# Optimization experiments

Measured on AMD Instinct MI355X. Metric: run time of the kernel, lower is better.

Reference implementation:

```python
import jax, jax.numpy as jnp
import numpy as np

N, E, F_IN, E_DIM, H, G = 8192, 40960, 32, 8, 64, 64
EPS = 1e-5


def _lin(key, fan_in, fan_out):
    k1, k2 = jax.random.split(key)
    s = 1.0 / np.sqrt(fan_in)
    w = jax.random.uniform(k1, (fan_in, fan_out), jnp.float32, -s, s)
    b = jax.random.uniform(k2, (fan_out,), jnp.float32, -s, s)
    return w, b


def setup_inputs() -> dict:
    key = jax.random.key(0)
    ks = jax.random.split(key, 32)
    inp = {}
    inp['x'] = jax.random.normal(ks[0], (N, F_IN), jnp.float32)
    inp['edge_index'] = jax.random.randint(ks[1], (2, E), 0, N)
    inp['edge_attr'] = jax.random.normal(ks[2], (E, E_DIM), jnp.float32)
    inp['batch'] = jnp.sort(jax.random.randint(ks[3], (N,), 0, G))
    # NNConv 1 (F_IN -> H)
    inp['e1_w1'], inp['e1_b1'] = _lin(ks[4], E_DIM, H)
    inp['e1_w2'], inp['e1_b2'] = _lin(ks[5], H, F_IN * H)
    inp['root1_w'], inp['root1_b'] = _lin(ks[6], F_IN, H)
    inp['bn1_g'] = jnp.ones((H,), jnp.float32); inp['bn1_b'] = jnp.zeros((H,), jnp.float32)
    # NNConv 2 (H -> H)
    inp['e2_w1'], inp['e2_b1'] = _lin(ks[7], E_DIM, H)
    inp['e2_w2'], inp['e2_b2'] = _lin(ks[8], H, H * H)
    inp['root2_w'], inp['root2_b'] = _lin(ks[9], H, H)
    inp['bn2_g'] = jnp.ones((H,), jnp.float32); inp['bn2_b'] = jnp.zeros((H,), jnp.float32)
    # NNConv 3 (H -> H)
    inp['e3_w1'], inp['e3_b1'] = _lin(ks[10], E_DIM, H)
    inp['e3_w2'], inp['e3_b2'] = _lin(ks[11], H, H * H)
    inp['root3_w'], inp['root3_b'] = _lin(ks[12], H, H)
    inp['bn3_g'] = jnp.ones((H,), jnp.float32); inp['bn3_b'] = jnp.zeros((H,), jnp.float32)
    # attention gate MLP: H -> H//2 -> 1
    inp['gate_w1'], inp['gate_b1'] = _lin(ks[13], H, H // 2)
    inp['gate_w2'], inp['gate_b2'] = _lin(ks[14], H // 2, 1)
    # fc head: H -> 2H (BN, relu) -> H (BN, relu) -> 1
    inp['fc1_w'], inp['fc1_b'] = _lin(ks[15], H, 2 * H)
    inp['fcbn1_g'] = jnp.ones((2 * H,), jnp.float32); inp['fcbn1_b'] = jnp.zeros((2 * H,), jnp.float32)
    inp['fc2_w'], inp['fc2_b'] = _lin(ks[16], 2 * H, H)
    inp['fcbn2_g'] = jnp.ones((H,), jnp.float32); inp['fcbn2_b'] = jnp.zeros((H,), jnp.float32)
    inp['fc3_w'], inp['fc3_b'] = _lin(ks[17], H, 1)
    return inp


def _bn(x, g, b):
    # training-mode batch norm over node/graph dim
    m = jnp.mean(x, axis=0)
    v = jnp.var(x, axis=0)
    return (x - m) * jax.lax.rsqrt(v + EPS) * g + b


def _nnconv(x, edge_index, edge_attr, w1, b1, w2, b2, root_w, root_b, in_ch, out_ch):
    src, dst = edge_index[0], edge_index[1]
    h = jax.nn.relu(edge_attr @ w1 + b1)                     # [E, H]
    We = (h @ w2 + b2).reshape(-1, in_ch, out_ch)            # [E, in, out]
    msg = jnp.einsum('ei,eio->eo', x[src], We)               # [E, out]
    s = jax.ops.segment_sum(msg, dst, num_segments=N)
    cnt = jax.ops.segment_sum(jnp.ones((msg.shape[0],), x.dtype), dst, num_segments=N)
    agg = s / jnp.clip(cnt, 1.0)[:, None]                    # mean aggregation
    return agg + x @ root_w + root_b


def _global_attention(x, batch, gw1, gb1, gw2, gb2):
    gate = jax.nn.relu(x @ gw1 + gb1) @ gw2 + gb2            # [N, 1]
    gate = gate[:, 0]
    m = jax.ops.segment_max(gate, batch, num_segments=G)
    e = jnp.exp(gate - m[batch])
    z = jax.ops.segment_sum(e, batch, num_segments=G)
    alpha = e / z[batch]
    return jax.ops.segment_sum(alpha[:, None] * x, batch, num_segments=G)  # [G, H]


def reference(x, edge_index, edge_attr, batch,
              e1_w1, e1_b1, e1_w2, e1_b2, root1_w, root1_b, bn1_g, bn1_b,
              e2_w1, e2_b1, e2_w2, e2_b2, root2_w, root2_b, bn2_g, bn2_b,
              e3_w1, e3_b1, e3_w2, e3_b2, root3_w, root3_b, bn3_g, bn3_b,
              gate_w1, gate_b1, gate_w2, gate_b2,
              fc1_w, fc1_b, fcbn1_g, fcbn1_b, fc2_w, fc2_b, fcbn2_g, fcbn2_b, fc3_w, fc3_b):
    x1 = jax.nn.relu(_bn(_nnconv(x, edge_index, edge_attr, e1_w1, e1_b1, e1_w2, e1_b2, root1_w, root1_b, F_IN, H), bn1_g, bn1_b))
    x2 = jax.nn.relu(_bn(_nnconv(x1, edge_index, edge_attr, e2_w1, e2_b1, e2_w2, e2_b2, root2_w, root2_b, H, H), bn2_g, bn2_b)) + x1
    x3 = jax.nn.relu(_bn(_nnconv(x2, edge_index, edge_attr, e3_w1, e3_b1, e3_w2, e3_b2, root3_w, root3_b, H, H), bn3_g, bn3_b)) + x2
    # dropout is identity in eval/reference mode
    p = _global_attention(x3, batch, gate_w1, gate_b1, gate_w2, gate_b2)  # [G, H]
    h = jax.nn.relu(_bn(p @ fc1_w + fc1_b, fcbn1_g, fcbn1_b))
    h = jax.nn.relu(_bn(h @ fc2_w + fc2_b, fcbn2_g, fcbn2_b))
    out = h @ fc3_w + fc3_b
    return out[:, 0]
```

## Files before the change

### kernel.cpp

```cpp
#include <hip/hip_runtime.h>
#include <hip/hip_bf16.h>

#define NN 8192
#define EE 40960
#define FIN 32
#define HH 64
#define GG 64

typedef __attribute__((ext_vector_type(4))) float f32x4;
typedef __attribute__((ext_vector_type(8))) short s16x8;
typedef unsigned short ushort_t;

__device__ __forceinline__ unsigned short f2bf(float f) {
    union { float f; unsigned int u; } v; v.f = f;
    unsigned int u = v.u;
    return (unsigned short)((u + 0x7fffu + ((u >> 16) & 1u)) >> 16);
}

__device__ __forceinline__ void gll16(const void* g, void* l) {
    __builtin_amdgcn_global_load_lds((__attribute__((address_space(1))) void*)g,
                                     (__attribute__((address_space(3))) void*)l, 16, 0, 0);
}

__global__ void btbuild_all_kernel(const float* __restrict__ w2a, const float* __restrict__ b2a, ushort_t* __restrict__ Bta,
                                   const float* __restrict__ w2b, const float* __restrict__ b2b, ushort_t* __restrict__ Btb,
                                   const float* __restrict__ w2c, const float* __restrict__ b2c, ushort_t* __restrict__ Btc,
                                   int* __restrict__ cnt, int* __restrict__ fill, float* __restrict__ stats,
                                   const float* __restrict__ x, const float* __restrict__ r1w,
                                   const float* __restrict__ r1b, float* __restrict__ rootbuf) {
    int bid = blockIdx.x;
    int t = threadIdx.x;

    if (bid >= 2600) {
        __shared__ float xs[16][36];
        __shared__ float rws[32 * 64];
        __shared__ float rbs[64];
        int blk = bid - 2600;
        for (int j = t; j < 512; j += 256) { int r = j >> 5, i = j & 31; xs[r][i] = x[(size_t)(blk * 16 + r) * 32 + i]; }
        for (int i = t; i < 2048; i += 256) rws[i] = r1w[i];
        if (t < 64) rbs[t] = r1b[t];
        __syncthreads();
        int r = t >> 4, cg = (t & 15) * 4;
        f32x4 s = *(const f32x4*)&rbs[cg];
#pragma unroll 8
        for (int i = 0; i < 32; i++) {
            float xv = xs[r][i];
            s += xv * (*(const f32x4*)&rws[i * 64 + cg]);
        }
        *(f32x4*)&rootbuf[(size_t)(blk * 16 + r) * 64 + cg] = s;
        return;
    }

    if (bid < 32) { cnt[bid * 256 + t] = 0; fill[bid * 256 + t] = 0; }
    if (bid == 32) stats[t] = 0.f;
    if (bid == 33 && t < 128) stats[256 + t] = 0.f;

    const float* w2; const float* b2; ushort_t* Bt; int IC; int base;
    if (bid < 520)       { w2 = w2a; b2 = b2a; Bt = Bta; IC = 32; base = bid; }
    else if (bid < 1560) { w2 = w2b; b2 = b2b; Bt = Btb; IC = 64; base = bid - 520; }
    else                 { w2 = w2c; b2 = b2c; Bt = Btc; IC = 64; base = bid - 1560; }
    int CH = IC >> 3;
    int flat = base * 256 + t;
    if (flat >= 64 * 65 * IC) return;
    int s = flat / (64 * IC);
    int rem = flat - s * (64 * IC);
    int row = rem / IC;
    int j = rem - row * IC;
    int q = j >> 3, w = j & 7;
    int c = q ^ (row & (CH - 1));
    int i = c * 8 + w;
    float v = (s < 64) ? w2[s * (IC * 64) + i * 64 + row] : b2[i * 64 + row];
    Bt[flat] = f2bf(v);
}

__global__ void hist_kernel(const int* __restrict__ dst, int* __restrict__ cnt) {
    int e = blockIdx.x * 256 + threadIdx.x;
    if (e < EE) atomicAdd(&cnt[dst[e]], 1);
}

__global__ void scan_kernel(const int* __restrict__ cnt, int* __restrict__ row_ptr) {
    __shared__ int lds[1024];
    int t = threadIdx.x;
    int v[8]; int s = 0;
    int base = t * 8;
#pragma unroll
    for (int j = 0; j < 8; j++) { v[j] = s; s += cnt[base + j]; }
    lds[t] = s;
    __syncthreads();
    for (int off = 1; off < 1024; off <<= 1) {
        int add = (t >= off) ? lds[t - off] : 0;
        __syncthreads();
        lds[t] += add;
        __syncthreads();
    }
    int ex = lds[t] - s;
#pragma unroll
    for (int j = 0; j < 8; j++) row_ptr[base + j] = ex + v[j];
    if (t == 1023) row_ptr[NN] = lds[1023];
}

__global__ void scatter_kernel(const int* __restrict__ dst, const int* __restrict__ row_ptr,
                               int* __restrict__ fill, int* __restrict__ perm) {
    int e = blockIdx.x * 256 + threadIdx.x;
    if (e < EE) {
        int d = dst[e];
        int pos = row_ptr[d] + atomicAdd(&fill[d], 1);
        perm[pos] = e;
    }
}

template<int IC>
__launch_bounds__(256, 5)
__global__ void conv_msg_kernel(const float* __restrict__ eattr,
                                const float* __restrict__ w1,
                                const float* __restrict__ b1,
                                const float* __restrict__ xin,
                                const int* __restrict__ src,
                                const int* __restrict__ perm,
                                const ushort_t* __restrict__ Bt,
                                float* __restrict__ msg) {
    constexpr int NKK  = IC / 32;
    constexpr int CH   = IC / 8;
    constexpr int TILE = IC * 64;
    constexpr int NQ   = (TILE * 2) / 4096;
    __shared__ ushort_t bt_lds[2][TILE];
    __shared__ float h_t[2048];
    __shared__ float ea_s[32][9];
    __shared__ float w1s[512];
    __shared__ float b1s[64];
    __shared__ int eid_s[32];

    const int t = threadIdx.x;
    const int wave = t >> 6;
    const int l = t & 63;
    const int g = l >> 4;
    const int rlo = l & 15;
    const int e0 = blockIdx.x * 32;

    auto stage = [&](int buf, int step) {
#pragma unroll
        for (int q = 0; q < NQ; ++q) {
            int off = q * 2048 + wave * 512;
            const ushort_t* gp = Bt + (size_t)step * TILE + off + l * 8;
            gll16(gp, &bt_lds[buf][off]);
        }
    };

    stage(0, 0);

    if (t < 32) eid_s[t] = perm[e0 + t];
    if (t < 64) b1s[t] = b1[t];
    for (int i = t; i < 512; i += 256) w1s[i] = w1[i];
    __syncthreads();

    { int e = t >> 3, i = t & 7; ea_s[e][i] = eattr[(size_t)eid_s[e] * 8 + i]; }

    s16x8 afrag[2][NKK];
#pragma unroll
    for (int m = 0; m < 2; ++m) {
        int row = m * 16 + rlo;
        int sn = src[eid_s[row]];
        const float* xp = xin + (size_t)sn * IC + g * 8;
#pragma unroll
        for (int kk = 0; kk < NKK; ++kk) {
            f32x4 a = *(const f32x4*)(xp + kk * 32);
            f32x4 b = *(const f32x4*)(xp + kk * 32 + 4);
            s16x8 fr;
            fr[0] = (short)f2bf(a[0]); fr[1] = (short)f2bf(a[1]);
            fr[2] = (short)f2bf(a[2]); fr[3] = (short)f2bf(a[3]);
            fr[4] = (short)f2bf(b[0]); fr[5] = (short)f2bf(b[1]);
            fr[6] = (short)f2bf(b[2]); fr[7] = (short)f2bf(b[3]);
            afrag[m][kk] = fr;
        }
    }
    __syncthreads();

#pragma unroll
    for (int j = 0; j < 8; ++j) {
        int idx = t + 256 * j;
        int k = idx >> 5, e = idx & 31;
        float s = b1s[k];
#pragma unroll
        for (int i = 0; i < 8; i++) s += ea_s[e][i] * w1s[i * 64 + k];
        h_t[idx] = fmaxf(s, 0.f);
    }
    __syncthreads();

    f32x4 acc[2];
#pragma unroll
    for (int m = 0; m < 2; m++) acc[m] = (f32x4){0.f, 0.f, 0.f, 0.f};

    const int bcol = wave * 16 + rlo;
    const int bmask = bcol & (CH - 1);
    const f32x4 zf = (f32x4){0.f, 0.f, 0.f, 0.f};

    for (int step = 0; step < 65; ++step) {
        if (step < 64) stage((step + 1) & 1, step + 1);
        const int buf = step & 1;
        s16x8 bfr[NKK];
#pragma unroll
        for (int kk = 0; kk < NKK; kk++) {
            int q = (kk * 4 + g) ^ bmask;
            bfr[kk] = *(const s16x8*)&bt_lds[buf][bcol * IC + q * 8];
        }
#pragma unroll
        for (int m = 0; m < 2; m++) {
            f32x4 P = __builtin_amdgcn_mfma_f32_16x16x32_bf16(afrag[m][0], bfr[0], zf, 0, 0, 0);
            if constexpr (NKK == 2)
                P = __builtin_amdgcn_mfma_f32_16x16x32_bf16(afrag[m][1], bfr[1], P, 0, 0, 0);
            if (step == 64) {
                acc[m] += P;
            } else {
                f32x4 h4 = *(const f32x4*)&h_t[(step << 5) + m * 16 + (g << 2)];
                acc[m] += h4 * P;
            }
        }
        __syncthreads();
    }

#pragma unroll
    for (int m = 0; m < 2; m++) {
        int row = e0 + m * 16 + (g << 2);
        float* mp = msg + (size_t)row * 64 + wave * 16 + rlo;
        mp[0] = acc[m][0]; mp[64] = acc[m][1]; mp[128] = acc[m][2]; mp[192] = acc[m][3];
    }
}

__global__ void aggregate_kernel(const float* __restrict__ msg, const int* __restrict__ row_ptr,
                                 const float* __restrict__ rootbuf,
                                 float* __restrict__ y, float* __restrict__ stats) {
    int t = threadIdx.x;
    int n = blockIdx.x * 16 + (t >> 4);
    int cg = (t & 15) * 4;
    int s = row_ptr[n], e = row_ptr[n + 1];
    f32x4 acc = (f32x4){0.f, 0.f, 0.f, 0.f};
    for (int j = s; j < e; ++j) {
        acc += *(const f32x4*)&msg[(size_t)j * 64 + cg];
    }
    float inv = 1.0f / fmaxf((float)(e - s), 1.0f);
    acc *= inv;
    acc += *(const f32x4*)&rootbuf[(size_t)n * 64 + cg];
    *(f32x4*)&y[(size_t)n * 64 + cg] = acc;

    f32x4 a2 = acc * acc;
#pragma unroll
    for (int j = 0; j < 4; j++) {
        acc[j] += __shfl_xor(acc[j], 16); acc[j] += __shfl_xor(acc[j], 32);
        a2[j]  += __shfl_xor(a2[j], 16);  a2[j]  += __shfl_xor(a2[j], 32);
    }
    __shared__ float ls[4][64], lq[4][64];
    int w = t >> 6;
    if ((t & 63) < 16) {
#pragma unroll
        for (int j = 0; j < 4; j++) { ls[w][cg + j] = acc[j]; lq[w][cg + j] = a2[j]; }
    }
    __syncthreads();
    if (t < 64) {
        float S = ls[0][t] + ls[1][t] + ls[2][t] + ls[3][t];
        float Q = lq[0][t] + lq[1][t] + lq[2][t] + lq[3][t];
        atomicAdd(&stats[t], S);
        atomicAdd(&stats[64 + t], Q);
    }
}

__global__ void bn_apply_root_kernel(const float* __restrict__ y, const float* __restrict__ stats,
                                     const float* __restrict__ gam, const float* __restrict__ bet,
                                     const float* __restrict__ res, float* __restrict__ xout,
                                     const float* __restrict__ rw, const float* __restrict__ rb,
                                     float* __restrict__ rootbuf) {
    __shared__ float xs[16][68];
    __shared__ float rws[64 * 64];
    __shared__ float rbs[64];
    int t = threadIdx.x;
    for (int i = t; i < 4096; i += 256) rws[i] = rw[i];
    if (t < 64) rbs[t] = rb[t];
    int i4 = blockIdx.x * 256 + t;
    int row = t >> 4, cg = (t & 15) * 4;
    const float invN = 1.0f / (float)NN;
    f32x4 yv = *(const f32x4*)&y[(size_t)i4 * 4];
    f32x4 o;
#pragma unroll
    for (int j = 0; j < 4; j++) {
        int c = cg + j;
        float mean = stats[c] * invN;
        float var = stats[64 + c] * invN - mean * mean;
        float sc = rsqrtf(var + 1e-5f) * gam[c];
        o[j] = fmaxf((yv[j] - mean) * sc + bet[c], 0.f);
    }
    if (res) o += *(const f32x4*)&res[(size_t)i4 * 4];
    *(f32x4*)&xout[(size_t)i4 * 4] = o;
    *(f32x4*)&xs[row][cg] = o;
    __syncthreads();
    f32x4 s = *(const f32x4*)&rbs[cg];
#pragma unroll 8
    for (int i = 0; i < 64; i++) {
        float xv = xs[row][i];
        s += xv * (*(const f32x4*)&rws[i * 64 + cg]);
    }
    *(f32x4*)&rootbuf[(size_t)(blockIdx.x * 16 + row) * 64 + cg] = s;
}

__global__ void bn_gate_kernel(const float* __restrict__ y, const float* __restrict__ stats,
                               const float* __restrict__ gam, const float* __restrict__ bet,
                               const float* __restrict__ res, float* __restrict__ xout,
                               const float* __restrict__ gw1, const float* __restrict__ gb1,
                               const float* __restrict__ gw2, const float* __restrict__ gb2,
                               float* __restrict__ gate) {
    __shared__ float x3s[64][68];
    __shared__ float w1s[2048];
    __shared__ float b1s[32], w2s[32];
    __shared__ float b2s;
    int t = threadIdx.x;
    for (int i = t; i < 2048; i += 256) w1s[i] = gw1[i];
    if (t < 32) { b1s[t] = gb1[t]; w2s[t] = gw2[t]; }
    if (t == 0) b2s = gb2[0];
    const float invN = 1.0f / (float)NN;
    size_t base4 = (size_t)blockIdx.x * 1024;
#pragma unroll
    for (int j = 0; j < 4; j++) {
        int i4l = j * 256 + t;
        int row = i4l >> 4, cg = (i4l & 15) * 4;
        f32x4 yv = *(const f32x4*)&y[(base4 + i4l) * 4];
        f32x4 o;
#pragma unroll
        for (int jj = 0; jj < 4; jj++) {
            int c = cg + jj;
            float mean = stats[c] * invN;
            float var = stats[64 + c] * invN - mean * mean;
            float sc = rsqrtf(var + 1e-5f) * gam[c];
            o[jj] = fmaxf((yv[jj] - mean) * sc + bet[c], 0.f);
        }
        o += *(const f32x4*)&res[(base4 + i4l) * 4];
        *(f32x4*)&xout[(base4 + i4l) * 4] = o;
        *(f32x4*)&x3s[row][cg] = o;
    }
    __syncthreads();
    int w = t >> 6, l = t & 63;
    int row = w * 16 + (l >> 2), part = l & 3;
    float hacc[8];
#pragma unroll
    for (int j = 0; j < 8; j++) hacc[j] = b1s[part * 8 + j];
    for (int i = 0; i < 64; i++) {
        float xv = x3s[row][i];
#pragma unroll
        for (int j = 0; j < 8; j++) hacc[j] += xv * w1s[i * 32 + part * 8 + j];
    }
    float gv = 0.f;
#pragma unroll
    for (int j = 0; j < 8; j++) gv += fmaxf(hacc[j], 0.f) * w2s[part * 8 + j];
    gv += __shfl_xor(gv, 1); gv += __shfl_xor(gv, 2);
    if (part == 0) gate[blockIdx.x * 64 + row] = gv + b2s;
}

__global__ void attn_pool_kernel(const float* __restrict__ x3, const float* __restrict__ gate,
                                 const int* __restrict__ batch, float* __restrict__ p) {
    int g = blockIdx.x;
    int t = threadIdx.x;
    int lo = 0, hi = NN;
    while (lo < hi) { int mid = (lo + hi) >> 1; if (batch[mid] < g) lo = mid + 1; else hi = mid; }
    int s = lo;
    hi = NN;
    while (lo < hi) { int mid = (lo + hi) >> 1; if (batch[mid] < g + 1) lo = mid + 1; else hi = mid; }
    int e = lo;

    __shared__ float red[4];
    __shared__ float sM, sZ;
    float m = -1e30f;
    for (int n = s + t; n < e; n += 256) m = fmaxf(m, gate[n]);
#pragma unroll
    for (int off = 1; off < 64; off <<= 1) m = fmaxf(m, __shfl_xor(m, off));
    if ((t & 63) == 0) red[t >> 6] = m;
    __syncthreads();
    if (t == 0) sM = fmaxf(fmaxf(red[0], red[1]), fmaxf(red[2], red[3]));
    __syncthreads();
    float z = 0.f;
    for (int n = s + t; n < e; n += 256) z += __expf(gate[n] - sM);
#pragma unroll
    for (int off = 1; off < 64; off <<= 1) z += __shfl_xor(z, off);
    if ((t & 63) == 0) red[t >> 6] = z;
    __syncthreads();
    if (t == 0) sZ = red[0] + red[1] + red[2] + red[3];
    __syncthreads();
    int w = t >> 6, c = t & 63;
    float acc = 0.f;
    for (int n = s + w; n < e; n += 4) acc += __expf(gate[n] - sM) * x3[(size_t)n * 64 + c];
    __shared__ float pa[4][64];
    pa[w][c] = acc;
    __syncthreads();
    if (t < 64) {
        float v = pa[0][t] + pa[1][t] + pa[2][t] + pa[3][t];
        p[g * 64 + t] = (sZ > 0.f) ? v / sZ : 0.f;
    }
}

__global__ void head1_kernel(const float* __restrict__ p, const float* __restrict__ fc1w,
                             const float* __restrict__ fc1b, const float* __restrict__ bn1g,
                             const float* __restrict__ bn1b, float* __restrict__ t1n) {
    __shared__ float sp[64 * 65];
    __shared__ float w1s[64 * 16];
    __shared__ float t1s[64 * 17];
    __shared__ float sA[16], sB[16];
    int t = threadIdx.x;
    int c0 = blockIdx.x * 16;
    for (int i = t; i < 4096; i += 256) { int r = i >> 6, cc = i & 63; sp[r * 65 + cc] = p[i]; }
    for (int i = t; i < 1024; i += 256) { int r = i >> 4, cc = i & 15; w1s[i] = fc1w[r * 128 + c0 + cc]; }
    __syncthreads();
    int r16 = t >> 4, c = t & 15;
    float b = fc1b[c0 + c];
#pragma unroll
    for (int rb = 0; rb < 4; rb++) {
        int row = rb * 16 + r16;
        float s = b;
#pragma unroll 8
        for (int i = 0; i < 64; i++) s += sp[row * 65 + i] * w1s[i * 16 + c];
        t1s[row * 17 + c] = s;
    }
    __syncthreads();
    if (t < 16) {
        float su = 0.f, sq = 0.f;
        for (int r = 0; r < 64; r++) { float v = t1s[r * 17 + t]; su += v; sq += v * v; }
        float mean = su * (1.f / 64.f), var = sq * (1.f / 64.f) - mean * mean;
        float sc = rsqrtf(var + 1e-5f) * bn1g[c0 + t];
        sA[t] = sc; sB[t] = bn1b[c0 + t] - mean * sc;
    }
    __syncthreads();
#pragma unroll
    for (int rb = 0; rb < 4; rb++) {
        int row = rb * 16 + r16;
        float v = t1s[row * 17 + c] * sA[c] + sB[c];
        t1n[row * 128 + c0 + c] = fmaxf(v, 0.f);
    }
}

__global__ void head2_kernel(const float* __restrict__ t1n, const float* __restrict__ fc2w,
                             const float* __restrict__ fc2b, const float* __restrict__ bn2g,
                             const float* __restrict__ bn2b, float* __restrict__ y2n) {
    __shared__ float t1sh[64 * 129];
    __shared__ float w2s[128 * 8];
    __shared__ float t2s[64 * 9];
    __shared__ float sA[8], sB[8];
    int t = threadIdx.x;
    int c0 = blockIdx.x * 8;
    for (int i = t; i < 8192; i += 256) { int r = i >> 7, cc = i & 127; t1sh[r * 129 + cc] = t1n[i]; }
    for (int i = t; i < 1024; i += 256) { int r = i >> 3, cc = i & 7; w2s[i] = fc2w[r * 64 + c0 + cc]; }
    __syncthreads();
    int r32 = t >> 3, c = t & 7;
    float b = fc2b[c0 + c];
#pragma unroll
    for (int rb = 0; rb < 2; rb++) {
        int row = rb * 32 + r32;
        float s = b;
#pragma unroll 8
        for (int i = 0; i < 128; i++) s += t1sh[row * 129 + i] * w2s[i * 8 + c];
        t2s[row * 9 + c] = s;
    }
    __syncthreads();
    if (t < 8) {
        float su = 0.f, sq = 0.f;
        for (int r = 0; r < 64; r++) { float v = t2s[r * 9 + t]; su += v; sq += v * v; }
        float mean = su * (1.f / 64.f), var = sq * (1.f / 64.f) - mean * mean;
        float sc = rsqrtf(var + 1e-5f) * bn2g[c0 + t];
        sA[t] = sc; sB[t] = bn2b[c0 + t] - mean * sc;
    }
    __syncthreads();
#pragma unroll
    for (int rb = 0; rb < 2; rb++) {
        int row = rb * 32 + r32;
        float v = t2s[row * 9 + c] * sA[c] + sB[c];
        y2n[row * 64 + c0 + c] = fmaxf(v, 0.f);
    }
}

__global__ void head3_kernel(const float* __restrict__ y2n, const float* __restrict__ fc3w,
                             const float* __restrict__ fc3b, float* __restrict__ out) {
    __shared__ float w3[64];
    int t = threadIdx.x;
    w3[t] = fc3w[t];
    __syncthreads();
    float s = fc3b[0];
    const float* yr = y2n + t * 64;
#pragma unroll 8
    for (int i = 0; i < 64; i++) s += yr[i] * w3[i];
    out[t] = s;
}

extern "C" void kernel_launch(void* const* d_in, const int* in_sizes, int n_in,
                              void* d_out, int out_size, void* d_ws, size_t ws_size,
                              hipStream_t stream) {
    const float* x     = (const float*)d_in[0];
    const int*   eidx  = (const int*)d_in[1];
    const float* eattr = (const float*)d_in[2];
    const int*   batch = (const int*)d_in[3];
    const float* e1w1 = (const float*)d_in[4];  const float* e1b1 = (const float*)d_in[5];
    const float* e1w2 = (const float*)d_in[6];  const float* e1b2 = (const float*)d_in[7];
    const float* r1w  = (const float*)d_in[8];  const float* r1b  = (const float*)d_in[9];
    const float* bn1g = (const float*)d_in[10]; const float* bn1b = (const float*)d_in[11];
    const float* e2w1 = (const float*)d_in[12]; const float* e2b1 = (const float*)d_in[13];
    const float* e2w2 = (const float*)d_in[14]; const float* e2b2 = (const float*)d_in[15];
    const float* r2w  = (const float*)d_in[16]; const float* r2b  = (const float*)d_in[17];
    const float* bn2g = (const float*)d_in[18]; const float* bn2b = (const float*)d_in[19];
    const float* e3w1 = (const float*)d_in[20]; const float* e3b1 = (const float*)d_in[21];
    const float* e3w2 = (const float*)d_in[22]; const float* e3b2 = (const float*)d_in[23];
    const float* r3w  = (const float*)d_in[24]; const float* r3b  = (const float*)d_in[25];
    const float* bn3g = (const float*)d_in[26]; const float* bn3b = (const float*)d_in[27];
    const float* gw1  = (const float*)d_in[28]; const float* gb1  = (const float*)d_in[29];
    const float* gw2  = (const float*)d_in[30]; const float* gb2  = (const float*)d_in[31];
    const float* fc1w = (const float*)d_in[32]; const float* fc1b = (const float*)d_in[33];
    const float* fbn1g= (const float*)d_in[34]; const float* fbn1b= (const float*)d_in[35];
    const float* fc2w = (const float*)d_in[36]; const float* fc2b = (const float*)d_in[37];
    const float* fbn2g= (const float*)d_in[38]; const float* fbn2b= (const float*)d_in[39];
    const float* fc3w = (const float*)d_in[40]; const float* fc3b = (const float*)d_in[41];
    float* out = (float*)d_out;

    const int* src = eidx;
    const int* dst = eidx + EE;

    char* ws = (char*)d_ws;
    size_t off = 0;
    auto take = [&](size_t n) { void* p = ws + off; off = (off + n + 255) & ~(size_t)255; return p; };
    ushort_t* Bt1 = (ushort_t*)take((size_t)65 * 2048 * 2);
    ushort_t* Bt2 = (ushort_t*)take((size_t)65 * 4096 * 2);
    ushort_t* Bt3 = (ushort_t*)take((size_t)65 * 4096 * 2);
    float* msg  = (float*)take((size_t)EE * 64 * 4);
    float* ybuf = (float*)take((size_t)NN * 64 * 4);
    float* x1   = (float*)take((size_t)NN * 64 * 4);
    float* x2   = (float*)take((size_t)NN * 64 * 4);
    float* x3   = (float*)take((size_t)NN * 64 * 4);
    float* rootbuf = (float*)take((size_t)NN * 64 * 4);
    float* gate = (float*)take((size_t)NN * 4);
    float* pbuf = (float*)take(64 * 64 * 4);
    float* t1n  = (float*)take(64 * 128 * 4);
    float* y2n  = (float*)take(64 * 64 * 4);
    float* stats = (float*)take(384 * 4);
    int* cnt  = (int*)take((size_t)NN * 4);
    int* fill = (int*)take((size_t)NN * 4);
    int* rowp = (int*)take((size_t)(NN + 1) * 4);
    int* perm = (int*)take((size_t)EE * 4);

    btbuild_all_kernel<<<3112, 256, 0, stream>>>(e1w2, e1b2, Bt1, e2w2, e2b2, Bt2,
                                                 e3w2, e3b2, Bt3, cnt, fill, stats,
                                                 x, r1w, r1b, rootbuf);
    hist_kernel<<<160, 256, 0, stream>>>(dst, cnt);
    scan_kernel<<<1, 1024, 0, stream>>>(cnt, rowp);
    scatter_kernel<<<160, 256, 0, stream>>>(dst, rowp, fill, perm);

    conv_msg_kernel<32><<<1280, 256, 0, stream>>>(eattr, e1w1, e1b1, x, src, perm, Bt1, msg);
    aggregate_kernel<<<512, 256, 0, stream>>>(msg, rowp, rootbuf, ybuf, stats);
    bn_apply_root_kernel<<<512, 256, 0, stream>>>(ybuf, stats, bn1g, bn1b, nullptr, x1,
                                                  r2w, r2b, rootbuf);

    conv_msg_kernel<64><<<1280, 256, 0, stream>>>(eattr, e2w1, e2b1, x1, src, perm, Bt2, msg);
    aggregate_kernel<<<512, 256, 0, stream>>>(msg, rowp, rootbuf, ybuf, stats + 128);
    bn_apply_root_kernel<<<512, 256, 0, stream>>>(ybuf, stats + 128, bn2g, bn2b, x1, x2,
                                                  r3w, r3b, rootbuf);

    conv_msg_kernel<64><<<1280, 256, 0, stream>>>(eattr, e3w1, e3b1, x2, src, perm, Bt3, msg);
    aggregate_kernel<<<512, 256, 0, stream>>>(msg, rowp, rootbuf, ybuf, stats + 256);
    bn_gate_kernel<<<128, 256, 0, stream>>>(ybuf, stats + 256, bn3g, bn3b, x2, x3,
                                            gw1, gb1, gw2, gb2, gate);

    attn_pool_kernel<<<64, 256, 0, stream>>>(x3, gate, batch, pbuf);
    head1_kernel<<<8, 256, 0, stream>>>(pbuf, fc1w, fc1b, fbn1g, fbn1b, t1n);
    head2_kernel<<<8, 256, 0, stream>>>(t1n, fc2w, fc2b, fbn2g, fbn2b, y2n);
    head3_kernel<<<1, 64, 0, stream>>>(y2n, fc3w, fc3b, out);
}
```

Before: 239.3 us.

## Stage two weight tiles per barrier in conv message kernel, rebuild Bt via LDS transpose

The conv message kernel now stages two consecutive B tiles per double-buffer phase, halving the number of barriers in the 65-step loop. It doubles LDS for the B buffers and shrinks the hidden-activation buffer by storing it as bf16, which adds a precision loss on the edge MLP output. Occupancy hints drop from 5 to 4 blocks. The weight-transpose build kernel now uses one block per slice with an LDS transpose for coalesced reads, and the Bt buffers are padded so the final phase's prefetch of the 66th tile stays in bounds.

```diff
diff --git a/kernel.cpp b/kernel.cpp
--- a/kernel.cpp
+++ b/kernel.cpp
@@ -9,12 +9,17 @@
 
 typedef __attribute__((ext_vector_type(4))) float f32x4;
 typedef __attribute__((ext_vector_type(8))) short s16x8;
+typedef __attribute__((ext_vector_type(4))) short s16x4;
 typedef unsigned short ushort_t;
 
 __device__ __forceinline__ unsigned short f2bf(float f) {
     union { float f; unsigned int u; } v; v.f = f;
     unsigned int u = v.u;
     return (unsigned short)((u + 0x7fffu + ((u >> 16) & 1u)) >> 16);
+}
+
+__device__ __forceinline__ float bf2f(unsigned short u) {
+    union { unsigned int i; float f; } v; v.i = ((unsigned)u) << 16; return v.f;
 }
 
 __device__ __forceinline__ void gll16(const void* g, void* l) {
@@ -31,11 +36,44 @@
     int bid = blockIdx.x;
     int t = threadIdx.x;
 
-    if (bid >= 2600) {
+    if (bid < 195) {
+        __shared__ float ws[64 * 65];
+        const float* w2; const float* b2; ushort_t* Bt; int IC, sh, s;
+        if (bid < 65)       { w2 = w2a; b2 = b2a; Bt = Bta; IC = 32; sh = 5; s = bid; }
+        else if (bid < 130) { w2 = w2b; b2 = b2b; Bt = Btb; IC = 64; sh = 6; s = bid - 65; }
+        else                { w2 = w2c; b2 = b2c; Bt = Btc; IC = 64; sh = 6; s = bid - 130; }
+        const int CH = IC >> 3;
+        const int NEL = IC * 64;
+        const float* src = (s < 64) ? (w2 + (size_t)s * NEL) : b2;
+        for (int idx = t; idx < NEL; idx += 256) {
+            int i = idx >> 6, o = idx & 63;
+            ws[i * 65 + o] = src[idx];
+        }
+        __syncthreads();
+        ushort_t* dst = Bt + (size_t)s * NEL;
+        for (int fl = t; fl < NEL; fl += 256) {
+            int row = fl >> sh;
+            int j = fl & (IC - 1);
+            int q = j >> 3, w = j & 7;
+            int c = q ^ (row & (CH - 1));
+            int i = c * 8 + w;
+            dst[fl] = f2bf(ws[i * 65 + row]);
+        }
+        return;
+    }
+    if (bid < 227) {
+        int b = bid - 195;
+        cnt[b * 256 + t] = 0; fill[b * 256 + t] = 0;
+        return;
+    }
+    if (bid == 227) { stats[t] = 0.f; return; }
+    if (bid == 228) { if (t < 128) stats[256 + t] = 0.f; return; }
+
+    {
         __shared__ float xs[16][36];
         __shared__ float rws[32 * 64];
         __shared__ float rbs[64];
-        int blk = bid - 2600;
+        int blk = bid - 229;
         for (int j = t; j < 512; j += 256) { int r = j >> 5, i = j & 31; xs[r][i] = x[(size_t)(blk * 16 + r) * 32 + i]; }
         for (int i = t; i < 2048; i += 256) rws[i] = r1w[i];
         if (t < 64) rbs[t] = r1b[t];
@@ -48,29 +86,7 @@
             s += xv * (*(const f32x4*)&rws[i * 64 + cg]);
         }
         *(f32x4*)&rootbuf[(size_t)(blk * 16 + r) * 64 + cg] = s;
-        return;
-    }
-
-    if (bid < 32) { cnt[bid * 256 + t] = 0; fill[bid * 256 + t] = 0; }
-    if (bid == 32) stats[t] = 0.f;
-    if (bid == 33 && t < 128) stats[256 + t] = 0.f;
-
-    const float* w2; const float* b2; ushort_t* Bt; int IC; int base;
-    if (bid < 520)       { w2 = w2a; b2 = b2a; Bt = Bta; IC = 32; base = bid; }
-    else if (bid < 1560) { w2 = w2b; b2 = b2b; Bt = Btb; IC = 64; base = bid - 520; }
-    else                 { w2 = w2c; b2 = b2c; Bt = Btc; IC = 64; base = bid - 1560; }
-    int CH = IC >> 3;
-    int flat = base * 256 + t;
-    if (flat >= 64 * 65 * IC) return;
-    int s = flat / (64 * IC);
-    int rem = flat - s * (64 * IC);
-    int row = rem / IC;
-    int j = rem - row * IC;
-    int q = j >> 3, w = j & 7;
-    int c = q ^ (row & (CH - 1));
-    int i = c * 8 + w;
-    float v = (s < 64) ? w2[s * (IC * 64) + i * 64 + row] : b2[i * 64 + row];
-    Bt[flat] = f2bf(v);
+    }
 }
 
 __global__ void hist_kernel(const int* __restrict__ dst, int* __restrict__ cnt) {
@@ -110,21 +126,21 @@
 }
 
 template<int IC>
-__launch_bounds__(256, 5)
-__global__ void conv_msg_kernel(const float* __restrict__ eattr,
-                                const float* __restrict__ w1,
-                                const float* __restrict__ b1,
-                                const float* __restrict__ xin,
-                                const int* __restrict__ src,
-                                const int* __restrict__ perm,
-                                const ushort_t* __restrict__ Bt,
-                                float* __restrict__ msg) {
+__launch_bounds__(256, 4)
+__global__ void conv_msg_pair_kernel(const float* __restrict__ eattr,
+                                     const float* __restrict__ w1,
+                                     const float* __restrict__ b1,
+                                     const float* __restrict__ xin,
+                                     const int* __restrict__ src,
+                                     const int* __restrict__ perm,
+                                     const ushort_t* __restrict__ Bt,
+                                     float* __restrict__ msg) {
     constexpr int NKK  = IC / 32;
     constexpr int CH   = IC / 8;
     constexpr int TILE = IC * 64;
-    constexpr int NQ   = (TILE * 2) / 4096;
-    __shared__ ushort_t bt_lds[2][TILE];
-    __shared__ float h_t[2048];
+    constexpr int NQT  = TILE / 2048;
+    __shared__ ushort_t bt_lds[2][2 * TILE];
+    __shared__ ushort_t h_t[2048];
     __shared__ float ea_s[32][9];
     __shared__ float w1s[512];
     __shared__ float b1s[64];
@@ -137,11 +153,11 @@
     const int rlo = l & 15;
     const int e0 = blockIdx.x * 32;
 
-    auto stage = [&](int buf, int step) {
-#pragma unroll
-        for (int q = 0; q < NQ; ++q) {
+    auto stage = [&](int buf, int phase) {
+#pragma unroll
+        for (int q = 0; q < 2 * NQT; ++q) {
             int off = q * 2048 + wave * 512;
-            const ushort_t* gp = Bt + (size_t)step * TILE + off + l * 8;
+            const ushort_t* gp = Bt + (size_t)(2 * phase) * TILE + off + l * 8;
             gll16(gp, &bt_lds[buf][off]);
         }
     };
@@ -182,7 +198,7 @@
         float s = b1s[k];
 #pragma unroll
         for (int i = 0; i < 8; i++) s += ea_s[e][i] * w1s[i * 64 + k];
-        h_t[idx] = fmaxf(s, 0.f);
+        h_t[idx] = f2bf(fmaxf(s, 0.f));
     }
     __syncthreads();
 
@@ -194,14 +210,12 @@
     const int bmask = bcol & (CH - 1);
     const f32x4 zf = (f32x4){0.f, 0.f, 0.f, 0.f};
 
-    for (int step = 0; step < 65; ++step) {
-        if (step < 64) stage((step + 1) & 1, step + 1);
-        const int buf = step & 1;
+    auto compute = [&](int buf, int sub, int step) {
         s16x8 bfr[NKK];
 #pragma unroll
         for (int kk = 0; kk < NKK; kk++) {
             int q = (kk * 4 + g) ^ bmask;
-            bfr[kk] = *(const s16x8*)&bt_lds[buf][bcol * IC + q * 8];
+            bfr[kk] = *(const s16x8*)&bt_lds[buf][sub * TILE + bcol * IC + q * 8];
         }
 #pragma unroll
         for (int m = 0; m < 2; m++) {
@@ -211,10 +225,22 @@
             if (step == 64) {
                 acc[m] += P;
             } else {
-                f32x4 h4 = *(const f32x4*)&h_t[(step << 5) + m * 16 + (g << 2)];
+                s16x4 hv = *(const s16x4*)&h_t[(step << 5) + m * 16 + (g << 2)];
+                f32x4 h4;
+                h4[0] = bf2f((unsigned short)hv[0]);
+                h4[1] = bf2f((unsigned short)hv[1]);
+                h4[2] = bf2f((unsigned short)hv[2]);
+                h4[3] = bf2f((unsigned short)hv[3]);
                 acc[m] += h4 * P;
             }
         }
+    };
+
+    for (int ph = 0; ph < 33; ++ph) {
+        if (ph < 32) stage((ph + 1) & 1, ph + 1);
+        const int buf = ph & 1;
+        compute(buf, 0, 2 * ph);
+        if (ph < 32) compute(buf, 1, 2 * ph + 1);
         __syncthreads();
     }
 
@@ -518,9 +544,9 @@
     char* ws = (char*)d_ws;
     size_t off = 0;
     auto take = [&](size_t n) { void* p = ws + off; off = (off + n + 255) & ~(size_t)255; return p; };
-    ushort_t* Bt1 = (ushort_t*)take((size_t)65 * 2048 * 2);
-    ushort_t* Bt2 = (ushort_t*)take((size_t)65 * 4096 * 2);
-    ushort_t* Bt3 = (ushort_t*)take((size_t)65 * 4096 * 2);
+    ushort_t* Bt1 = (ushort_t*)take((size_t)66 * 2048 * 2);
+    ushort_t* Bt2 = (ushort_t*)take((size_t)66 * 4096 * 2);
+    ushort_t* Bt3 = (ushort_t*)take((size_t)66 * 4096 * 2);
     float* msg  = (float*)take((size_t)EE * 64 * 4);
     float* ybuf = (float*)take((size_t)NN * 64 * 4);
     float* x1   = (float*)take((size_t)NN * 64 * 4);
@@ -537,24 +563,24 @@
     int* rowp = (int*)take((size_t)(NN + 1) * 4);
     int* perm = (int*)take((size_t)EE * 4);
 
-    btbuild_all_kernel<<<3112, 256, 0, stream>>>(e1w2, e1b2, Bt1, e2w2, e2b2, Bt2,
-                                                 e3w2, e3b2, Bt3, cnt, fill, stats,
-                                                 x, r1w, r1b, rootbuf);
+    btbuild_all_kernel<<<741, 256, 0, stream>>>(e1w2, e1b2, Bt1, e2w2, e2b2, Bt2,
+                                                e3w2, e3b2, Bt3, cnt, fill, stats,
+                                                x, r1w, r1b, rootbuf);
     hist_kernel<<<160, 256, 0, stream>>>(dst, cnt);
     scan_kernel<<<1, 1024, 0, stream>>>(cnt, rowp);
     scatter_kernel<<<160, 256, 0, stream>>>(dst, rowp, fill, perm);
 
-    conv_msg_kernel<32><<<1280, 256, 0, stream>>>(eattr, e1w1, e1b1, x, src, perm, Bt1, msg);
+    conv_msg_pair_kernel<32><<<1280, 256, 0, stream>>>(eattr, e1w1, e1b1, x, src, perm, Bt1, msg);
     aggregate_kernel<<<512, 256, 0, stream>>>(msg, rowp, rootbuf, ybuf, stats);
     bn_apply_root_kernel<<<512, 256, 0, stream>>>(ybuf, stats, bn1g, bn1b, nullptr, x1,
                                                   r2w, r2b, rootbuf);
 
-    conv_msg_kernel<64><<<1280, 256, 0, stream>>>(eattr, e2w1, e2b1, x1, src, perm, Bt2, msg);
+    conv_msg_pair_kernel<64><<<1280, 256, 0, stream>>>(eattr, e2w1, e2b1, x1, src, perm, Bt2, msg);
     aggregate_kernel<<<512, 256, 0, stream>>>(msg, rowp, rootbuf, ybuf, stats + 128);
     bn_apply_root_kernel<<<512, 256, 0, stream>>>(ybuf, stats + 128, bn2g, bn2b, x1, x2,
                                                   r3w, r3b, rootbuf);
 
-    conv_msg_kernel<64><<<1280, 256, 0, stream>>>(eattr, e3w1, e3b1, x2, src, perm, Bt3, msg);
+    conv_msg_pair_kernel<64><<<1280, 256, 0, stream>>>(eattr, e3w1, e3b1, x2, src, perm, Bt3, msg);
     aggregate_kernel<<<512, 256, 0, stream>>>(msg, rowp, rootbuf, ybuf, stats + 256);
     bn_gate_kernel<<<128, 256, 0, stream>>>(ybuf, stats + 256, bn3g, bn3b, x2, x3,
                                             gw1, gb1, gw2, gb2, gate);
```

Result: no change. 243.4 us (+1.7%).
